# Kernel tuning notes

Hardware: AMD Instinct MI355X
Metric: run time of the kernel (lower is better)

Reference implementation:

```python
import jax, jax.numpy as jnp
import numpy as np

GAMMA = 1.1

B, T, N, M, F = 2, 8, 65536, 128, 5
NUM_SAMPLE = 128


def setup_inputs() -> dict:
    key = jax.random.key(0)
    k1, k2, k3 = jax.random.split(key, 3)
    # Points already split per (batch, frame), as produced by the time-mask filter in the original forward.
    points = jax.random.normal(k1, (B, T, N, F), dtype=jnp.float32)
    # Boxes: [x, y, z, l, w, h, ry]; centers/extents in [0,1) so radii ~0.4 and some points fall inside.
    trajectory_rois = jax.random.uniform(k2, (B, T, M, 7), dtype=jnp.float32)
    valid_length = jax.random.randint(k3, (B, T, M), 0, 2)
    return {
        "points": points,
        "trajectory_rois": trajectory_rois,
        "valid_length": valid_length,
        "num_sample": NUM_SAMPLE,
    }


def _cylindrical_pool(pts, boxes, num_sample):
    # pts: [N, F], boxes: [M, 7]
    radii = jnp.linalg.norm(boxes[:, 3:5] * 0.5, axis=-1) * GAMMA          # [M]
    dis = jnp.linalg.norm(pts[None, :, :2] - boxes[:, None, :2], axis=-1)  # [M, N]
    point_mask = (dis <= radii[:, None]).astype(pts.dtype)                 # [M, N]
    sampled_mask, sampled_idx = jax.lax.top_k(point_mask, num_sample)      # [M, S]
    sampled = pts[sampled_idx]                                             # [M, S, F] gather
    return jnp.where(sampled_mask[..., None] > 0, sampled, 0.0)


def reference(points, trajectory_rois, valid_length, num_sample):
    # points: [B, T, N, F], trajectory_rois: [B, T, M, 7], valid_length: [B, T, M]
    pool = lambda p, b: _cylindrical_pool(p, b, num_sample)
    key_points = jax.vmap(jax.vmap(pool))(points, trajectory_rois)  # [B, T, M, S, F]
    # For frames idx != 0 with valid_length == 0, fall back to the frame-0 sampled points.
    # (The subsequent in-place xy shift in the torch code writes into a temporary copy and is a no-op;
    #  we faithfully replicate the no-op.)
    t_idx = jnp.arange(key_points.shape[1])
    cond = (valid_length == 0) & (t_idx[None, :, None] != 0)        # [B, T, M]
    key_points = jnp.where(cond[..., None, None], key_points[:, :1], key_points)
    # stack -> permute(0,2,1,3,4) -> flatten(2,3)
    out = jnp.transpose(key_points, (0, 2, 1, 3, 4))                # [B, M, T, S, F]
    b, m, t, s, f = out.shape
    return out.reshape(b, m, t * s, f)
```

## Files before the change

### kernel.cpp

```cpp
#include <hip/hip_runtime.h>

using u64 = unsigned long long;

constexpr int Bc = 2, Tc = 8, Fc = 5, Mc = 128, Sc = 128;
constexpr int Np = 65536;
constexpr int WPTS = 512;
constexpr int NCH = Np / WPTS;
constexpr int NR  = NCH / 4;

__device__ __forceinline__ float sqrt_ub(float r) {
    float u = __fmul_rn(r, r);
    if (__fsqrt_rn(u) <= r) {
        while (true) {
            float nu = __uint_as_float(__float_as_uint(u) + 1u);
            if (__fsqrt_rn(nu) <= r) u = nu; else break;
        }
    } else {
        while (__fsqrt_rn(u) > r) u = __uint_as_float(__float_as_uint(u) - 1u);
    }
    return u;
}

__device__ __forceinline__ float box_radius(const float* __restrict__ box) {
    const float hl = __fmul_rn(0.5f, box[3]);
    const float hw = __fmul_rn(0.5f, box[4]);
    return __fmul_rn(__fsqrt_rn(__fadd_rn(__fmul_rn(hl, hl), __fmul_rn(hw, hw))), 1.1f);
}

__global__ __launch_bounds__(256) void k_box(
    const float* __restrict__ points,
    const float* __restrict__ rois,
    const int*   __restrict__ vlen,
    float*       __restrict__ out)
{
    const int blk = blockIdx.x;
    const int m  = blk & (Mc - 1);
    const int bt = blk >> 7;
    const int t = bt & 7, b = bt >> 3;

    int t_eff = t;
    if (t != 0 && vlen[bt * Mc + m] == 0) t_eff = 0;
    const int btE = b * Tc + t_eff;

    const float* box = rois + (size_t)(btE * Mc + m) * 7;
    const float cx = box[0], cy = box[1];
    const float T = sqrt_ub(box_radius(box));
    const float* pts = points + (size_t)btE * Np * Fc;
    float* orow = out + (size_t)((b * Mc + m) * Tc + t) * (Sc * Fc);

    __shared__ int wcnt[2][4];

    const int tid = threadIdx.x, lane = tid & 63, wv = tid >> 6;
    const u64 lt = (1ull << lane) - 1ull;

    float px[8], py[8];
    {
        const int pbase = wv * WPTS;
        #pragma unroll
        for (int i = 0; i < 8; ++i) {
            const size_t idx = (size_t)(pbase + i * 64 + lane);
            px[i] = pts[idx * Fc + 0];
            py[i] = pts[idx * Fc + 1];
        }
    }

    int cum = 0;
    for (int r = 0; r < NR; ++r) {
        u64 bal[8];
        int c = 0;
        #pragma unroll
        for (int i = 0; i < 8; ++i) {
            const float dx = __fsub_rn(px[i], cx);
            const float dy = __fsub_rn(py[i], cy);
            const float d2 = __fadd_rn(__fmul_rn(dx, dx), __fmul_rn(dy, dy));
            bal[i] = __ballot(d2 <= T);
            c += (int)__popcll(bal[i]);
        }
        if (lane == 0) wcnt[r & 1][wv] = c;

        float nx[8], ny[8];
        if (r + 1 < NR) {
            const int pbase = ((r + 1) * 4 + wv) * WPTS;
            #pragma unroll
            for (int i = 0; i < 8; ++i) {
                const size_t idx = (size_t)(pbase + i * 64 + lane);
                nx[i] = pts[idx * Fc + 0];
                ny[i] = pts[idx * Fc + 1];
            }
        }

        __syncthreads();
        const int c0 = wcnt[r & 1][0], c1 = wcnt[r & 1][1];
        const int c2 = wcnt[r & 1][2], c3 = wcnt[r & 1][3];
        int base = cum;
        if (wv > 0) base += c0;
        if (wv > 1) base += c1;
        if (wv > 2) base += c2;
        const int tot = c0 + c1 + c2 + c3;

        if (base < Sc && c > 0) {
            const int pbase = (r * 4 + wv) * WPTS;
            int sb = base;
            #pragma unroll
            for (int i = 0; i < 8; ++i) {
                const bool inside = (bal[i] >> lane) & 1ull;
                if (inside) {
                    const int slot = sb + (int)__popcll(bal[i] & lt);
                    if (slot < Sc) {
                        const size_t idx = (size_t)(pbase + i * 64 + lane);
                        float* o = orow + (size_t)slot * Fc;
                        o[0] = px[i]; o[1] = py[i];
                        o[2] = pts[idx * Fc + 2];
                        o[3] = pts[idx * Fc + 3];
                        o[4] = pts[idx * Fc + 4];
                    }
                }
                sb += (int)__popcll(bal[i]);
            }
        }

        cum += tot;
        if (cum >= Sc) break;
        #pragma unroll
        for (int i = 0; i < 8; ++i) { px[i] = nx[i]; py[i] = ny[i]; }
    }

    const int fill = min(cum, Sc);
    for (int i = fill * Fc + tid; i < Sc * Fc; i += 256) orow[i] = 0.0f;
}

__global__ __launch_bounds__(1024) void vox_pool(
    const float* __restrict__ points, const float* __restrict__ rois,
    const int* __restrict__ valid_length, float* __restrict__ out,
    int N, int M, int S)
{
    const int blk = blockIdx.x;
    const int m = blk % M;
    const int t = (blk / M) % Tc;
    const int b = blk / (M * Tc);
    int t_eff = t;
    if (t != 0 && valid_length[(b * Tc + t) * M + m] == 0) t_eff = 0;
    const float* box = rois + (size_t)((b * Tc + t_eff) * M + m) * 7;
    const float cx = box[0], cy = box[1];
    const float r = box_radius(box);
    const float* pts = points + (size_t)(b * Tc + t_eff) * N * Fc;
    float* o = out + ((size_t)(b * M + m) * Tc + t) * (size_t)S * Fc;
    __shared__ int wcnt[16];
    const int tid = threadIdx.x, lane = tid & 63, wav = tid >> 6;
    const int nthreads = blockDim.x, nwaves = nthreads >> 6;
    int cnt = 0;
    for (int basei = 0; basei < N; basei += nthreads) {
        const int idx = basei + tid;
        bool inside = false;
        if (idx < N) {
            const float dx = __fsub_rn(pts[(size_t)idx * Fc + 0], cx);
            const float dy = __fsub_rn(pts[(size_t)idx * Fc + 1], cy);
            const float d2 = __fadd_rn(__fmul_rn(dx, dx), __fmul_rn(dy, dy));
            inside = (__fsqrt_rn(d2) <= r);
        }
        const unsigned long long bal = __ballot(inside);
        if (lane == 0) wcnt[wav] = __popcll(bal);
        __syncthreads();
        int wave_off = 0, block_tot = 0;
        for (int w = 0; w < nwaves; ++w) {
            const int c = wcnt[w];
            if (w < wav) wave_off += c;
            block_tot += c;
        }
        if (inside) {
            const int slot = cnt + wave_off + (int)__popcll(bal & ((1ull << lane) - 1ull));
            if (slot < S)
                for (int f = 0; f < Fc; ++f)
                    o[(size_t)slot * Fc + f] = pts[(size_t)idx * Fc + f];
        }
        cnt += block_tot;
        __syncthreads();
        if (cnt >= S) break;
    }
    const int filled = cnt < S ? cnt : S;
    for (int s = filled + tid; s < S; s += nthreads)
        for (int f = 0; f < Fc; ++f)
            o[(size_t)s * Fc + f] = 0.0f;
}

extern "C" void kernel_launch(void* const* d_in, const int* in_sizes, int n_in,
                              void* d_out, int out_size, void* d_ws, size_t ws_size,
                              hipStream_t stream) {
    const float* points = (const float*)d_in[0];
    const float* rois   = (const float*)d_in[1];
    const int*   vlen   = (const int*)d_in[2];
    float* out = (float*)d_out;

    const bool fixed =
        in_sizes[0] == Bc * Tc * Np * Fc &&
        in_sizes[1] == Bc * Tc * Mc * 7 &&
        in_sizes[2] == Bc * Tc * Mc &&
        out_size    == Bc * Mc * Tc * Sc * Fc;

    if (fixed) {
        k_box<<<dim3(Bc * Tc * Mc), 256, 0, stream>>>(points, rois, vlen, out);
    } else {
        const int N = in_sizes[0] / (Bc * Tc * Fc);
        const int M = in_sizes[2] / (Bc * Tc);
        const int S = out_size / (Bc * M * Tc * Fc);
        vox_pool<<<dim3(Bc * Tc * M), 1024, 0, stream>>>(points, rois, vlen, out, N, M, S);
    }
}
```

Measured before the change: 54.46 us.

## Deepen point prefetch to two rounds and use a lighter LDS-only barrier

```diff
diff --git a/kernel.cpp b/kernel.cpp
--- a/kernel.cpp
+++ b/kernel.cpp
@@ -25,6 +25,12 @@
     const float hl = __fmul_rn(0.5f, box[3]);
     const float hw = __fmul_rn(0.5f, box[4]);
     return __fmul_rn(__fsqrt_rn(__fadd_rn(__fmul_rn(hl, hl), __fmul_rn(hw, hw))), 1.1f);
+}
+
+__device__ __forceinline__ void light_barrier() {
+    asm volatile("s_waitcnt lgkmcnt(0)" ::: "memory");
+    __builtin_amdgcn_s_barrier();
+    asm volatile("" ::: "memory");
 }
 
 __global__ __launch_bounds__(256) void k_box(
@@ -53,14 +59,21 @@
     const int tid = threadIdx.x, lane = tid & 63, wv = tid >> 6;
     const u64 lt = (1ull << lane) - 1ull;
 
-    float px[8], py[8];
+    float px[8], py[8], ax[8], ay[8];
     {
-        const int pbase = wv * WPTS;
-        #pragma unroll
-        for (int i = 0; i < 8; ++i) {
-            const size_t idx = (size_t)(pbase + i * 64 + lane);
-            px[i] = pts[idx * Fc + 0];
-            py[i] = pts[idx * Fc + 1];
+        const int p0 = wv * WPTS;
+        const int p1 = (4 + wv) * WPTS;
+        #pragma unroll
+        for (int i = 0; i < 8; ++i) {
+            const size_t i0 = (size_t)(p0 + i * 64 + lane);
+            px[i] = pts[i0 * Fc + 0];
+            py[i] = pts[i0 * Fc + 1];
+        }
+        #pragma unroll
+        for (int i = 0; i < 8; ++i) {
+            const size_t i1 = (size_t)(p1 + i * 64 + lane);
+            ax[i] = pts[i1 * Fc + 0];
+            ay[i] = pts[i1 * Fc + 1];
         }
     }
 
@@ -78,33 +91,36 @@
         }
         if (lane == 0) wcnt[r & 1][wv] = c;
 
-        float nx[8], ny[8];
-        if (r + 1 < NR) {
-            const int pbase = ((r + 1) * 4 + wv) * WPTS;
-            #pragma unroll
-            for (int i = 0; i < 8; ++i) {
-                const size_t idx = (size_t)(pbase + i * 64 + lane);
-                nx[i] = pts[idx * Fc + 0];
-                ny[i] = pts[idx * Fc + 1];
-            }
-        }
-
-        __syncthreads();
+        light_barrier();
+
         const int c0 = wcnt[r & 1][0], c1 = wcnt[r & 1][1];
         const int c2 = wcnt[r & 1][2], c3 = wcnt[r & 1][3];
         int base = cum;
         if (wv > 0) base += c0;
         if (wv > 1) base += c1;
         if (wv > 2) base += c2;
-        const int tot = c0 + c1 + c2 + c3;
+        const int newcum = cum + c0 + c1 + c2 + c3;
+
+        float fx[8], fy[8];
+        if (newcum < Sc && r + 2 < NR) {
+            const int pf = ((r + 2) * 4 + wv) * WPTS;
+            #pragma unroll
+            for (int i = 0; i < 8; ++i) {
+                const size_t idx = (size_t)(pf + i * 64 + lane);
+                fx[i] = pts[idx * Fc + 0];
+                fy[i] = pts[idx * Fc + 1];
+            }
+        } else {
+            #pragma unroll
+            for (int i = 0; i < 8; ++i) { fx[i] = 0.0f; fy[i] = 0.0f; }
+        }
 
         if (base < Sc && c > 0) {
             const int pbase = (r * 4 + wv) * WPTS;
             int sb = base;
             #pragma unroll
             for (int i = 0; i < 8; ++i) {
-                const bool inside = (bal[i] >> lane) & 1ull;
-                if (inside) {
+                if ((bal[i] >> lane) & 1ull) {
                     const int slot = sb + (int)__popcll(bal[i] & lt);
                     if (slot < Sc) {
                         const size_t idx = (size_t)(pbase + i * 64 + lane);
@@ -119,10 +135,13 @@
             }
         }
 
-        cum += tot;
+        cum = newcum;
         if (cum >= Sc) break;
         #pragma unroll
-        for (int i = 0; i < 8; ++i) { px[i] = nx[i]; py[i] = ny[i]; }
+        for (int i = 0; i < 8; ++i) {
+            px[i] = ax[i]; py[i] = ay[i];
+            ax[i] = fx[i]; ay[i] = fy[i];
+        }
     }
 
     const int fill = min(cum, Sc);
```

New measurement: 60.62 us. 11.3% more time.

## Split points into per-wave quarters with count pass then scatter pass

Applied to the files above, without the earlier changes.

```diff
diff --git a/kernel.cpp b/kernel.cpp
--- a/kernel.cpp
+++ b/kernel.cpp
@@ -1,12 +1,13 @@
 #include <hip/hip_runtime.h>
 
+using u16 = unsigned short;
 using u64 = unsigned long long;
 
 constexpr int Bc = 2, Tc = 8, Fc = 5, Mc = 128, Sc = 128;
 constexpr int Np = 65536;
-constexpr int WPTS = 512;
-constexpr int NCH = Np / WPTS;
-constexpr int NR  = NCH / 4;
+constexpr int QPTS = Np / 4;
+constexpr int IPTS = 512;
+constexpr int QITERS = QPTS / IPTS;
 
 __device__ __forceinline__ float sqrt_ub(float r) {
     float u = __fmul_rn(r, r);
@@ -48,84 +49,98 @@
     const float* pts = points + (size_t)btE * Np * Fc;
     float* orow = out + (size_t)((b * Mc + m) * Tc + t) * (Sc * Fc);
 
-    __shared__ int wcnt[2][4];
+    __shared__ int s_wcnt[4];
+    __shared__ int s_iters[4];
+    __shared__ u16 s_cnt[4][QITERS];
 
     const int tid = threadIdx.x, lane = tid & 63, wv = tid >> 6;
     const u64 lt = (1ull << lane) - 1ull;
 
-    float px[8], py[8];
-    {
-        const int pbase = wv * WPTS;
+    int c = 0;
+    int it = 0;
+    while (it < QITERS) {
+        const int pbase = wv * QPTS + it * IPTS;
+        int cc = 0;
         #pragma unroll
-        for (int i = 0; i < 8; ++i) {
-            const size_t idx = (size_t)(pbase + i * 64 + lane);
-            px[i] = pts[idx * Fc + 0];
-            py[i] = pts[idx * Fc + 1];
-        }
-    }
-
-    int cum = 0;
-    for (int r = 0; r < NR; ++r) {
-        u64 bal[8];
-        int c = 0;
-        #pragma unroll
-        for (int i = 0; i < 8; ++i) {
-            const float dx = __fsub_rn(px[i], cx);
-            const float dy = __fsub_rn(py[i], cy);
-            const float d2 = __fadd_rn(__fmul_rn(dx, dx), __fmul_rn(dy, dy));
-            bal[i] = __ballot(d2 <= T);
-            c += (int)__popcll(bal[i]);
-        }
-        if (lane == 0) wcnt[r & 1][wv] = c;
-
-        float nx[8], ny[8];
-        if (r + 1 < NR) {
-            const int pbase = ((r + 1) * 4 + wv) * WPTS;
+        for (int h = 0; h < 2; ++h) {
+            const float4* src = (const float4*)(pts + (size_t)(pbase + h * 256 + lane * 4) * Fc);
+            const float4 v0 = src[0], v1 = src[1], v2 = src[2], v3 = src[3], v4 = src[4];
+            const float qx0 = v0.x, qy0 = v0.y;
+            const float qx1 = v1.y, qy1 = v1.z;
+            const float qx2 = v2.z, qy2 = v2.w;
+            const float qx3 = v3.w, qy3 = v4.x;
             #pragma unroll
-            for (int i = 0; i < 8; ++i) {
-                const size_t idx = (size_t)(pbase + i * 64 + lane);
-                nx[i] = pts[idx * Fc + 0];
-                ny[i] = pts[idx * Fc + 1];
+            for (int k = 0; k < 4; ++k) {
+                const float qx = k == 0 ? qx0 : k == 1 ? qx1 : k == 2 ? qx2 : qx3;
+                const float qy = k == 0 ? qy0 : k == 1 ? qy1 : k == 2 ? qy2 : qy3;
+                const float dx = __fsub_rn(qx, cx);
+                const float dy = __fsub_rn(qy, cy);
+                const float d2 = __fadd_rn(__fmul_rn(dx, dx), __fmul_rn(dy, dy));
+                cc += (int)__popcll(__ballot(d2 <= T));
             }
         }
-
-        __syncthreads();
-        const int c0 = wcnt[r & 1][0], c1 = wcnt[r & 1][1];
-        const int c2 = wcnt[r & 1][2], c3 = wcnt[r & 1][3];
-        int base = cum;
-        if (wv > 0) base += c0;
-        if (wv > 1) base += c1;
-        if (wv > 2) base += c2;
-        const int tot = c0 + c1 + c2 + c3;
-
-        if (base < Sc && c > 0) {
-            const int pbase = (r * 4 + wv) * WPTS;
-            int sb = base;
+        if (lane == 0) s_cnt[wv][it] = (u16)cc;
+        c += cc;
+        ++it;
+        if (c >= Sc) break;
+    }
+    if (lane == 0) { s_wcnt[wv] = c < Sc ? c : Sc; s_iters[wv] = it; }
+
+    __syncthreads();
+
+    const int c0 = s_wcnt[0], c1 = s_wcnt[1], c2 = s_wcnt[2], c3 = s_wcnt[3];
+    const int total = c0 + c1 + c2 + c3;
+    int base = 0;
+    if (wv > 0) base += c0;
+    if (wv > 1) base += c1;
+    if (wv > 2) base += c2;
+    const int myiters = s_iters[wv];
+
+    if (base < Sc) {
+        int slot = base;
+        for (int i2 = 0; i2 < myiters && slot < Sc; ++i2) {
+            const int cc = (int)s_cnt[wv][i2];
+            if (cc == 0) continue;
+            const int pbase = wv * QPTS + i2 * IPTS;
+            int sb = slot;
             #pragma unroll
-            for (int i = 0; i < 8; ++i) {
-                const bool inside = (bal[i] >> lane) & 1ull;
-                if (inside) {
-                    const int slot = sb + (int)__popcll(bal[i] & lt);
-                    if (slot < Sc) {
-                        const size_t idx = (size_t)(pbase + i * 64 + lane);
-                        float* o = orow + (size_t)slot * Fc;
-                        o[0] = px[i]; o[1] = py[i];
-                        o[2] = pts[idx * Fc + 2];
-                        o[3] = pts[idx * Fc + 3];
-                        o[4] = pts[idx * Fc + 4];
+            for (int h = 0; h < 2; ++h) {
+                const float4* src = (const float4*)(pts + (size_t)(pbase + h * 256 + lane * 4) * Fc);
+                const float4 v0 = src[0], v1 = src[1], v2 = src[2], v3 = src[3], v4 = src[4];
+                float f[20];
+                *(float4*)&f[0]  = v0; *(float4*)&f[4]  = v1; *(float4*)&f[8]  = v2;
+                *(float4*)&f[12] = v3; *(float4*)&f[16] = v4;
+                u64 bal[4];
+                int below = 0, toth = 0;
+                #pragma unroll
+                for (int k = 0; k < 4; ++k) {
+                    const float dx = __fsub_rn(f[5 * k + 0], cx);
+                    const float dy = __fsub_rn(f[5 * k + 1], cy);
+                    const float d2 = __fadd_rn(__fmul_rn(dx, dx), __fmul_rn(dy, dy));
+                    bal[k] = __ballot(d2 <= T);
+                    below += (int)__popcll(bal[k] & lt);
+                    toth  += (int)__popcll(bal[k]);
+                }
+                int ownpre = 0;
+                #pragma unroll
+                for (int k = 0; k < 4; ++k) {
+                    if ((bal[k] >> lane) & 1ull) {
+                        const int sk = sb + below + ownpre;
+                        if (sk < Sc) {
+                            float* o = orow + (size_t)sk * Fc;
+                            o[0] = f[5*k+0]; o[1] = f[5*k+1]; o[2] = f[5*k+2];
+                            o[3] = f[5*k+3]; o[4] = f[5*k+4];
+                        }
+                        ++ownpre;
                     }
                 }
-                sb += (int)__popcll(bal[i]);
+                sb += toth;
             }
-        }
-
-        cum += tot;
-        if (cum >= Sc) break;
-        #pragma unroll
-        for (int i = 0; i < 8; ++i) { px[i] = nx[i]; py[i] = ny[i]; }
-    }
-
-    const int fill = min(cum, Sc);
+            slot = sb;
+        }
+    }
+
+    const int fill = total < Sc ? total : Sc;
     for (int i = fill * Fc + tid; i < Sc * Fc; i += 256) orow[i] = 0.0f;
 }
 
```

Result: slower. 122.0 us (+124.0%).

## Replace per-round block sync with two-pass count-then-scatter and early exit

Applied to the files above, without the earlier changes.

```diff
diff --git a/kernel.cpp b/kernel.cpp
--- a/kernel.cpp
+++ b/kernel.cpp
@@ -1,12 +1,14 @@
 #include <hip/hip_runtime.h>
 
+using u16 = unsigned short;
+using u32 = unsigned int;
 using u64 = unsigned long long;
 
 constexpr int Bc = 2, Tc = 8, Fc = 5, Mc = 128, Sc = 128;
 constexpr int Np = 65536;
-constexpr int WPTS = 512;
-constexpr int NCH = Np / WPTS;
-constexpr int NR  = NCH / 4;
+constexpr int CPTS = 512;
+constexpr int NCHK = Np / CPTS;
+constexpr int NB = 31;
 
 __device__ __forceinline__ float sqrt_ub(float r) {
     float u = __fmul_rn(r, r);
@@ -34,8 +36,8 @@
     float*       __restrict__ out)
 {
     const int blk = blockIdx.x;
-    const int m  = blk & (Mc - 1);
-    const int bt = blk >> 7;
+    const int bt = blk & 15;
+    const int m  = blk >> 4;
     const int t = bt & 7, b = bt >> 3;
 
     int t_eff = t;
@@ -48,64 +50,173 @@
     const float* pts = points + (size_t)btE * Np * Fc;
     float* orow = out + (size_t)((b * Mc + m) * Tc + t) * (Sc * Fc);
 
-    __shared__ int wcnt[2][4];
+    __shared__ u16 s_cnt[NCHK];
 
     const int tid = threadIdx.x, lane = tid & 63, wv = tid >> 6;
     const u64 lt = (1ull << lane) - 1ull;
 
-    float px[8], py[8];
+    float pxA[8], pyA[8];
     {
-        const int pbase = wv * WPTS;
+        const int pbase = wv * CPTS;
         #pragma unroll
         for (int i = 0; i < 8; ++i) {
             const size_t idx = (size_t)(pbase + i * 64 + lane);
-            px[i] = pts[idx * Fc + 0];
-            py[i] = pts[idx * Fc + 1];
-        }
-    }
-
-    int cum = 0;
-    for (int r = 0; r < NR; ++r) {
-        u64 bal[8];
-        int c = 0;
+            pxA[i] = pts[idx * Fc + 0];
+            pyA[i] = pts[idx * Fc + 1];
+        }
+    }
+    u64 balA[8]; int cA = 0;
+    #pragma unroll
+    for (int i = 0; i < 8; ++i) {
+        const float dx = __fsub_rn(pxA[i], cx);
+        const float dy = __fsub_rn(pyA[i], cy);
+        const float d2 = __fadd_rn(__fmul_rn(dx, dx), __fmul_rn(dy, dy));
+        balA[i] = __ballot(d2 <= T);
+        cA += (int)__popcll(balA[i]);
+    }
+    if (lane == 0) s_cnt[wv] = (u16)cA;
+    __syncthreads();
+
+    const int c0 = s_cnt[0], c1 = s_cnt[1], c2 = s_cnt[2], c3 = s_cnt[3];
+    const int cum4 = c0 + c1 + c2 + c3;
+    int baseA = 0;
+    if (wv > 0) baseA += c0;
+    if (wv > 1) baseA += c1;
+    if (wv > 2) baseA += c2;
+
+    if (cum4 >= Sc) {
+        if (baseA < Sc && cA > 0) {
+            int sb = baseA;
+            const int pbase = wv * CPTS;
+            #pragma unroll
+            for (int i = 0; i < 8; ++i) {
+                if ((balA[i] >> lane) & 1ull) {
+                    const int slot = sb + (int)__popcll(balA[i] & lt);
+                    if (slot < Sc) {
+                        const size_t idx = (size_t)(pbase + i * 64 + lane);
+                        float* o = orow + (size_t)slot * Fc;
+                        o[0] = pxA[i]; o[1] = pyA[i];
+                        o[2] = pts[idx * Fc + 2];
+                        o[3] = pts[idx * Fc + 3];
+                        o[4] = pts[idx * Fc + 4];
+                    }
+                }
+                sb += (int)__popcll(balA[i]);
+            }
+        }
+        return;
+    }
+
+    {
+        float px[8], py[8];
+        {
+            const int pbase = (4 + wv) * CPTS;
+            #pragma unroll
+            for (int i = 0; i < 8; ++i) {
+                const size_t idx = (size_t)(pbase + i * 64 + lane);
+                px[i] = pts[idx * Fc + 0];
+                py[i] = pts[idx * Fc + 1];
+            }
+        }
+        for (int j = 0; j < NB; ++j) {
+            float nx[8], ny[8];
+            if (j + 1 < NB) {
+                const int pbase = (4 + 4 * (j + 1) + wv) * CPTS;
+                #pragma unroll
+                for (int i = 0; i < 8; ++i) {
+                    const size_t idx = (size_t)(pbase + i * 64 + lane);
+                    nx[i] = pts[idx * Fc + 0];
+                    ny[i] = pts[idx * Fc + 1];
+                }
+            }
+            int cc = 0;
+            #pragma unroll
+            for (int i = 0; i < 8; ++i) {
+                const float dx = __fsub_rn(px[i], cx);
+                const float dy = __fsub_rn(py[i], cy);
+                const float d2 = __fadd_rn(__fmul_rn(dx, dx), __fmul_rn(dy, dy));
+                cc += (int)__popcll(__ballot(d2 <= T));
+            }
+            if (lane == 0) s_cnt[4 + 4 * j + wv] = (u16)cc;
+            if (j + 1 < NB) {
+                #pragma unroll
+                for (int i = 0; i < 8; ++i) { px[i] = nx[i]; py[i] = ny[i]; }
+            }
+        }
+    }
+    __syncthreads();
+
+    const u32 two = ((const u32*)s_cnt)[lane];
+    const int av  = (int)(two & 0xFFFFu);
+    const int av2 = (int)(two >> 16);
+    const int ssum = av + av2;
+    int incl = ssum;
+    #pragma unroll
+    for (int d = 1; d < 64; d <<= 1) { int v = __shfl_up(incl, d); if (lane >= d) incl += v; }
+    const int excl  = incl - ssum;
+    const int total = __shfl(incl, 63);
+
+    const int okv = (wv & 1) ? (excl + av) : excl;
+    const u64 okb = __ballot(okv < Sc);
+    const u64 wvmask = (wv < 2) ? 0x5555555555555554ull : 0xAAAAAAAAAAAAAAA8ull;
+    const int jcap = (int)__popcll(okb & wvmask);
+
+    if (cA > 0) {
+        int sb = baseA;
+        const int pbase = wv * CPTS;
         #pragma unroll
         for (int i = 0; i < 8; ++i) {
-            const float dx = __fsub_rn(px[i], cx);
-            const float dy = __fsub_rn(py[i], cy);
-            const float d2 = __fadd_rn(__fmul_rn(dx, dx), __fmul_rn(dy, dy));
-            bal[i] = __ballot(d2 <= T);
-            c += (int)__popcll(bal[i]);
-        }
-        if (lane == 0) wcnt[r & 1][wv] = c;
-
-        float nx[8], ny[8];
-        if (r + 1 < NR) {
-            const int pbase = ((r + 1) * 4 + wv) * WPTS;
-            #pragma unroll
-            for (int i = 0; i < 8; ++i) {
+            if ((balA[i] >> lane) & 1ull) {
+                const int slot = sb + (int)__popcll(balA[i] & lt);
                 const size_t idx = (size_t)(pbase + i * 64 + lane);
-                nx[i] = pts[idx * Fc + 0];
-                ny[i] = pts[idx * Fc + 1];
-            }
-        }
-
-        __syncthreads();
-        const int c0 = wcnt[r & 1][0], c1 = wcnt[r & 1][1];
-        const int c2 = wcnt[r & 1][2], c3 = wcnt[r & 1][3];
-        int base = cum;
-        if (wv > 0) base += c0;
-        if (wv > 1) base += c1;
-        if (wv > 2) base += c2;
-        const int tot = c0 + c1 + c2 + c3;
-
-        if (base < Sc && c > 0) {
-            const int pbase = (r * 4 + wv) * WPTS;
-            int sb = base;
-            #pragma unroll
-            for (int i = 0; i < 8; ++i) {
-                const bool inside = (bal[i] >> lane) & 1ull;
+                float* o = orow + (size_t)slot * Fc;
+                o[0] = pxA[i]; o[1] = pyA[i];
+                o[2] = pts[idx * Fc + 2];
+                o[3] = pts[idx * Fc + 3];
+                o[4] = pts[idx * Fc + 4];
+            }
+            sb += (int)__popcll(balA[i]);
+        }
+    }
+
+    if (jcap > 0) {
+        float px[8], py[8];
+        {
+            const int pbase = (4 + wv) * CPTS;
+            #pragma unroll
+            for (int i = 0; i < 8; ++i) {
+                const size_t idx = (size_t)(pbase + i * 64 + lane);
+                px[i] = pts[idx * Fc + 0];
+                py[i] = pts[idx * Fc + 1];
+            }
+        }
+        for (int j = 0; j < jcap; ++j) {
+            float nx[8], ny[8];
+            if (j + 1 < jcap) {
+                const int pbase = (4 + 4 * (j + 1) + wv) * CPTS;
+                #pragma unroll
+                for (int i = 0; i < 8; ++i) {
+                    const size_t idx = (size_t)(pbase + i * 64 + lane);
+                    nx[i] = pts[idx * Fc + 0];
+                    ny[i] = pts[idx * Fc + 1];
+                }
+            }
+            const int c = 4 + 4 * j + wv;
+            const int sl = c >> 1;
+            int bc = __shfl(excl, sl);
+            if (c & 1) bc += __shfl(av, sl);
+
+            const int pbase = c * CPTS;
+            int sb = bc;
+            #pragma unroll
+            for (int i = 0; i < 8; ++i) {
+                const float dx = __fsub_rn(px[i], cx);
+                const float dy = __fsub_rn(py[i], cy);
+                const float d2 = __fadd_rn(__fmul_rn(dx, dx), __fmul_rn(dy, dy));
+                const bool inside = (d2 <= T);
+                const u64 bal = __ballot(inside);
                 if (inside) {
-                    const int slot = sb + (int)__popcll(bal[i] & lt);
+                    const int slot = sb + (int)__popcll(bal & lt);
                     if (slot < Sc) {
                         const size_t idx = (size_t)(pbase + i * 64 + lane);
                         float* o = orow + (size_t)slot * Fc;
@@ -115,17 +226,16 @@
                         o[4] = pts[idx * Fc + 4];
                     }
                 }
-                sb += (int)__popcll(bal[i]);
-            }
-        }
-
-        cum += tot;
-        if (cum >= Sc) break;
-        #pragma unroll
-        for (int i = 0; i < 8; ++i) { px[i] = nx[i]; py[i] = ny[i]; }
-    }
-
-    const int fill = min(cum, Sc);
+                sb += (int)__popcll(bal);
+            }
+            if (j + 1 < jcap) {
+                #pragma unroll
+                for (int i = 0; i < 8; ++i) { px[i] = nx[i]; py[i] = ny[i]; }
+            }
+        }
+    }
+
+    const int fill = total < Sc ? total : Sc;
     for (int i = fill * Fc + tid; i < Sc * Fc; i += 256) orow[i] = 0.0f;
 }
 
```

After: 88.97 us. 63.4% more time.
